# Kernel tuning notes

Measured on AMD Instinct MI355X. Metric: run time of the kernel, lower is better.

The kernel has to match this reference:

```python
import jax, jax.numpy as jnp
import numpy as np
import math

B, H, L, D = 2, 16, 2048, 128


def setup_inputs() -> dict:
    key = jax.random.key(0)
    kq, kk, kv, km, kp = jax.random.split(key, 5)
    q = jax.random.normal(kq, (B, H, L, D), dtype=jnp.float32)
    k = jax.random.normal(kk, (B, H, L, D), dtype=jnp.float32)
    v = jax.random.normal(kv, (B, H, L, D), dtype=jnp.float32)
    mask = jax.random.randint(km, (B, 1, L, L), 0, 2, dtype=jnp.int32)
    probs = jax.random.uniform(kp, (B, L, L), dtype=jnp.float32)
    alpha = jnp.ones((), dtype=jnp.float32)  # learned scalar Parameter, init 1.0
    return {"q": q, "k": k, "v": v, "mask": mask, "probs": probs, "alpha": alpha}


def reference(q, k, v, mask, probs, alpha):
    # scores: (B, H, L, L)
    scale = 1.0 / math.sqrt(q.shape[-1])
    attn_score = jnp.einsum("bhqd,bhkd->bhqk", q, k) * scale
    # additive learned-scale probability bias, broadcast over heads
    attn_score = attn_score + probs[:, None, :, :] * alpha
    # masked_fill(mask == 0, -inf)
    attn_score = jnp.where(mask == 0, -jnp.inf, attn_score)
    attn_p = jax.nn.softmax(attn_score, axis=-1)
    # dropout p=0.0 -> identity
    attention = jnp.einsum("bhqk,bhkd->bhqd", attn_p, v)
    return attention, attn_p
```

## Files before the change

### kernel.cpp

```cpp
#include <hip/hip_runtime.h>

constexpr int BB = 2, HH = 16, LL = 2048, DD = 128;
constexpr int QB = 64, KB = 32, NKT = LL / KB;
constexpr float SCALE = 0.08838834764831845f;

typedef __attribute__((ext_vector_type(8))) short bf16x8;
typedef __attribute__((ext_vector_type(8))) unsigned short u16x8;
typedef __attribute__((ext_vector_type(4))) float f32x4;
typedef __attribute__((ext_vector_type(4))) int i32x4;

static __device__ __forceinline__ unsigned short f2bf(float f) {
  unsigned int u = __builtin_bit_cast(unsigned int, f);
  u += 0x7fffu + ((u >> 16) & 1u);
  return (unsigned short)(u >> 16);
}
static __device__ __forceinline__ float bf2f(unsigned short h) {
  return __builtin_bit_cast(float, (unsigned int)h << 16);
}

#define GLD16(gsrc, ldst) __builtin_amdgcn_global_load_lds( \
    (const __attribute__((address_space(1))) void*)(gsrc), \
    (__attribute__((address_space(3))) void*)(ldst), 16, 0, 0)

__global__ __launch_bounds__(256)
void prep_kernel(const float* __restrict__ k, const float* __restrict__ v,
                 const int* __restrict__ mask, const float* __restrict__ probs,
                 const float* __restrict__ alphap,
                 unsigned short* __restrict__ kbT, unsigned short* __restrict__ vtT,
                 unsigned short* __restrict__ cpw)
{
  __shared__ unsigned short sT[128 * 40];
  const int bid = blockIdx.x;
  const int bh = bid >> 6, kt = bid & 63;
  const int t = threadIdx.x;
  const float alpha = alphap[0];
  const size_t tileBase = (size_t)bid * 4096;
  const float* kg = k + ((size_t)bh * LL + kt * 32) * DD;
  const float* vg = v + ((size_t)bh * LL + kt * 32) * DD;

  #pragma unroll
  for (int s = t; s < 512; s += 256) {
    int dsl = s >> 5, key = s & 31;
    const float* src = kg + key * DD + dsl * 8;
    float4 a = *(const float4*)src;
    float4 c = *(const float4*)(src + 4);
    u16x8 w;
    w[0] = f2bf(a.x); w[1] = f2bf(a.y); w[2] = f2bf(a.z); w[3] = f2bf(a.w);
    w[4] = f2bf(c.x); w[5] = f2bf(c.y); w[6] = f2bf(c.z); w[7] = f2bf(c.w);
    *(u16x8*)(kbT + tileBase + (size_t)s * 8) = w;
  }
  #pragma unroll
  for (int i = 0; i < 4; ++i) {
    int idx = i * 256 + t;
    int key = idx >> 5, d4 = (idx & 31) * 4;
    float4 x = ((const float4*)vg)[idx];
    sT[(d4 + 0) * 40 + key] = f2bf(x.x);
    sT[(d4 + 1) * 40 + key] = f2bf(x.y);
    sT[(d4 + 2) * 40 + key] = f2bf(x.z);
    sT[(d4 + 3) * 40 + key] = f2bf(x.w);
  }
  {
    const float4* ps = (const float4*)probs;
    const int4* ms = (const int4*)mask;
    ushort4* cs = (ushort4*)cpw;
    size_t base = (size_t)bid * 1024;
    #pragma unroll
    for (int i = 0; i < 4; ++i) {
      size_t idx = base + i * 256 + t;
      float4 p = ps[idx];
      int4 m = ms[idx];
      ushort4 o;
      o.x = f2bf(m.x ? p.x * alpha : -1e30f);
      o.y = f2bf(m.y ? p.y * alpha : -1e30f);
      o.z = f2bf(m.z ? p.z * alpha : -1e30f);
      o.w = f2bf(m.w ? p.w * alpha : -1e30f);
      cs[idx] = o;
    }
  }
  __syncthreads();
  #pragma unroll
  for (int s = t; s < 512; s += 256) {
    int kc = s >> 7, d = s & 127;
    u16x8 w = *(const u16x8*)&sT[d * 40 + kc * 8];
    *(u16x8*)(vtT + tileBase + (size_t)s * 8) = w;
  }
}

__global__ __launch_bounds__(256, 4)
void attn_kernel(const float* __restrict__ q, const unsigned short* __restrict__ kbT,
                 const unsigned short* __restrict__ vtT, const unsigned short* __restrict__ cpw,
                 float* __restrict__ outA, float* __restrict__ outP)
{
  __shared__ unsigned short sK[2][4096];
  __shared__ unsigned short sVt[2][4096];

  const int tid = threadIdx.x;
  const int lane = tid & 63;
  const int wid = tid >> 6;
  const int l15 = lane & 15;
  const int l4 = lane >> 4;

  const int bid = blockIdx.x;
  const int work = ((bid & 7) << 7) | (bid >> 3);
  const int bh = work >> 5;
  const int qt = work & 31;
  const int b = bh >> 4;
  const int q0 = qt * QB;
  const int row16 = wid << 4;

  const unsigned short* kbh = kbT + (size_t)bh * 64 * 4096;
  const unsigned short* vbh = vtT + (size_t)bh * 64 * 4096;
  const unsigned short* cgrow = cpw + (size_t)b * LL * LL + (size_t)(q0 + row16 + l15) * LL;
  float* oA = outA + (size_t)(bh * LL + q0) * DD;
  float* oPr = outP + (size_t)bh * LL * LL + (size_t)(q0 + row16 + l15) * LL;

  bf16x8 qf0, qf1, qf2, qf3;
  {
    const float* qs = q + (size_t)(bh * LL + q0 + row16 + l15) * DD + l4 * 8;
    #define LQ(FR, KC) { \
      float4 a = *(const float4*)(qs + (KC) * 32); \
      float4 c = *(const float4*)(qs + (KC) * 32 + 4); \
      FR[0]=(short)f2bf(a.x); FR[1]=(short)f2bf(a.y); FR[2]=(short)f2bf(a.z); FR[3]=(short)f2bf(a.w); \
      FR[4]=(short)f2bf(c.x); FR[5]=(short)f2bf(c.y); FR[6]=(short)f2bf(c.z); FR[7]=(short)f2bf(c.w); }
    LQ(qf0, 0) LQ(qf1, 1) LQ(qf2, 2) LQ(qf3, 3)
    #undef LQ
  }

  #define DMA_K(BUF, KT) do { \
    GLD16(kbh + (size_t)(KT) * 4096 + tid * 8,         &sK[BUF][wid << 9]); \
    GLD16(kbh + (size_t)(KT) * 4096 + (256 + tid) * 8, &sK[BUF][2048 + (wid << 9)]); } while (0)
  #define DMA_V(BUF, KT) do { \
    GLD16(vbh + (size_t)(KT) * 4096 + tid * 8,         &sVt[BUF][wid << 9]); \
    GLD16(vbh + (size_t)(KT) * 4096 + (256 + tid) * 8, &sVt[BUF][2048 + (wid << 9)]); } while (0)

  #define QKS(KC, QF) { \
    bf16x8 k0 = *(const bf16x8*)&sK[cur][(((KC) * 4 + l4) * 32 + l15) * 8]; \
    a0 = __builtin_amdgcn_mfma_f32_16x16x32_bf16(k0, QF, a0, 0, 0, 0); \
    bf16x8 k1 = *(const bf16x8*)&sK[cur][(((KC) * 4 + l4) * 32 + 16 + l15) * 8]; \
    a1 = __builtin_amdgcn_mfma_f32_16x16x32_bf16(k1, QF, a1, 0, 0, 0); }

  DMA_K(0, 0);
  ushort4 cn0 = *(const ushort4*)(cgrow + (l4 << 2));
  ushort4 cn1 = *(const ushort4*)(cgrow + 16 + (l4 << 2));
  float sum = 0.f;
  for (int kt = 0; kt < NKT; ++kt) {
    const int cur = kt & 1;
    __syncthreads();
    if (kt + 1 < NKT) DMA_K(cur ^ 1, kt + 1);
    ushort4 b0 = cn0, b1 = cn1;
    if (kt + 1 < NKT) {
      cn0 = *(const ushort4*)(cgrow + (kt + 1) * 32 + (l4 << 2));
      cn1 = *(const ushort4*)(cgrow + (kt + 1) * 32 + 16 + (l4 << 2));
    }
    f32x4 a0 = {0.f,0.f,0.f,0.f}, a1 = {0.f,0.f,0.f,0.f};
    QKS(0, qf0) QKS(1, qf1) QKS(2, qf2) QKS(3, qf3)
    sum += __expf(a0[0] * SCALE + bf2f(b0.x));
    sum += __expf(a0[1] * SCALE + bf2f(b0.y));
    sum += __expf(a0[2] * SCALE + bf2f(b0.z));
    sum += __expf(a0[3] * SCALE + bf2f(b0.w));
    sum += __expf(a1[0] * SCALE + bf2f(b1.x));
    sum += __expf(a1[1] * SCALE + bf2f(b1.y));
    sum += __expf(a1[2] * SCALE + bf2f(b1.z));
    sum += __expf(a1[3] * SCALE + bf2f(b1.w));
  }
  sum += __shfl_xor(sum, 16, 64);
  sum += __shfl_xor(sum, 32, 64);
  const float inv = 1.0f / sum;

  __syncthreads();
  DMA_K(0, 0); DMA_V(0, 0);
  cn0 = *(const ushort4*)(cgrow + (l4 << 2));
  cn1 = *(const ushort4*)(cgrow + 16 + (l4 << 2));
  f32x4 oacc[8];
  #pragma unroll
  for (int dt = 0; dt < 8; ++dt) oacc[dt] = (f32x4){0.f,0.f,0.f,0.f};

  const int srcA = l15 + (((l4 << 1) + 0) & 3) * 16;
  const int srcB = l15 + (((l4 << 1) + 1) & 3) * 16;
  const bool hiTile = (l4 >= 2);

  for (int kt = 0; kt < NKT; ++kt) {
    const int cur = kt & 1;
    __syncthreads();
    if (kt + 1 < NKT) { DMA_K(cur ^ 1, kt + 1); DMA_V(cur ^ 1, kt + 1); }
    ushort4 b0 = cn0, b1 = cn1;
    if (kt + 1 < NKT) {
      cn0 = *(const ushort4*)(cgrow + (kt + 1) * 32 + (l4 << 2));
      cn1 = *(const ushort4*)(cgrow + (kt + 1) * 32 + 16 + (l4 << 2));
    }
    f32x4 a0 = {0.f,0.f,0.f,0.f}, a1 = {0.f,0.f,0.f,0.f};
    QKS(0, qf0) QKS(1, qf1) QKS(2, qf2) QKS(3, qf3)

    f32x4 p0, p1;
    p0[0] = __expf(a0[0] * SCALE + bf2f(b0.x)) * inv;
    p0[1] = __expf(a0[1] * SCALE + bf2f(b0.y)) * inv;
    p0[2] = __expf(a0[2] * SCALE + bf2f(b0.z)) * inv;
    p0[3] = __expf(a0[3] * SCALE + bf2f(b0.w)) * inv;
    p1[0] = __expf(a1[0] * SCALE + bf2f(b1.x)) * inv;
    p1[1] = __expf(a1[1] * SCALE + bf2f(b1.y)) * inv;
    p1[2] = __expf(a1[2] * SCALE + bf2f(b1.z)) * inv;
    p1[3] = __expf(a1[3] * SCALE + bf2f(b1.w)) * inv;

    __builtin_nontemporal_store(p0, (f32x4*)(oPr + kt * 32 + (l4 << 2)));
    __builtin_nontemporal_store(p1, (f32x4*)(oPr + kt * 32 + 16 + (l4 << 2)));

    unsigned d00, d01, d10, d11;
    asm("v_cvt_pk_bf16_f32 %0, %1, %2" : "=v"(d00) : "v"(p0[0]), "v"(p0[1]));
    asm("v_cvt_pk_bf16_f32 %0, %1, %2" : "=v"(d01) : "v"(p0[2]), "v"(p0[3]));
    asm("v_cvt_pk_bf16_f32 %0, %1, %2" : "=v"(d10) : "v"(p1[0]), "v"(p1[1]));
    asm("v_cvt_pk_bf16_f32 %0, %1, %2" : "=v"(d11) : "v"(p1[2]), "v"(p1[3]));
    int a00 = __shfl((int)d00, srcA, 64);
    int a01 = __shfl((int)d01, srcA, 64);
    int a02 = __shfl((int)d00, srcB, 64);
    int a03 = __shfl((int)d01, srcB, 64);
    int b00 = __shfl((int)d10, srcA, 64);
    int b01 = __shfl((int)d11, srcA, 64);
    int b02 = __shfl((int)d10, srcB, 64);
    int b03 = __shfl((int)d11, srcB, 64);
    i32x4 fw;
    fw[0] = hiTile ? b00 : a00;
    fw[1] = hiTile ? b01 : a01;
    fw[2] = hiTile ? b02 : a02;
    fw[3] = hiTile ? b03 : a03;
    bf16x8 aP = __builtin_bit_cast(bf16x8, fw);

    #pragma unroll
    for (int dt = 0; dt < 8; ++dt) {
      bf16x8 bV = *(const bf16x8*)&sVt[cur][(l4 * 128 + dt * 16 + l15) * 8];
      oacc[dt] = __builtin_amdgcn_mfma_f32_16x16x32_bf16(aP, bV, oacc[dt], 0, 0, 0);
    }
  }

  #pragma unroll
  for (int dt = 0; dt < 8; ++dt) {
    #pragma unroll
    for (int r = 0; r < 4; ++r) {
      __builtin_nontemporal_store(oacc[dt][r],
          oA + (size_t)(row16 + (l4 << 2) + r) * DD + dt * 16 + l15);
    }
  }
}

extern "C" void kernel_launch(void* const* d_in, const int* in_sizes, int n_in,
                              void* d_out, int out_size, void* d_ws, size_t ws_size,
                              hipStream_t stream) {
  const float* q = (const float*)d_in[0];
  const float* k = (const float*)d_in[1];
  const float* v = (const float*)d_in[2];
  const int* mask = (const int*)d_in[3];
  const float* probs = (const float*)d_in[4];
  const float* alpha = (const float*)d_in[5];
  float* outA = (float*)d_out;
  float* outP = outA + (size_t)BB * HH * LL * DD;
  unsigned short* kbT = (unsigned short*)d_ws;
  unsigned short* vtT = kbT + (size_t)32 * 64 * 4096;
  unsigned short* cpw = vtT + (size_t)32 * 64 * 4096;
  hipLaunchKernelGGL(prep_kernel, dim3(32 * 64), dim3(256), 0, stream,
                     k, v, mask, probs, alpha, kbT, vtT, cpw);
  hipLaunchKernelGGL(attn_kernel, dim3(BB * HH * (LL / QB)), dim3(256), 0, stream,
                     q, kbT, vtT, cpw, outA, outP);
}
```

Measured before the change: 286.4 us.

## Split attention into separate row-sum pass and output pass kernels

Splits the fused two-pass attention kernel into two launches. The first computes softmax denominators from QK^T only, using less shared memory and a higher occupancy bound, and writes the inverse sums to workspace. The second reloads them and runs the probability and PV pass. This lets the lighter first pass run at higher occupancy, at the cost of an extra launch, reloading and reconverting Q, and a small extra global write and read.

Result: faster. 280.3 us (-2.1%).

```diff
diff --git a/kernel.cpp b/kernel.cpp
--- a/kernel.cpp
+++ b/kernel.cpp
@@ -86,13 +86,11 @@
   }
 }
 
-__global__ __launch_bounds__(256, 4)
-void attn_kernel(const float* __restrict__ q, const unsigned short* __restrict__ kbT,
-                 const unsigned short* __restrict__ vtT, const unsigned short* __restrict__ cpw,
-                 float* __restrict__ outA, float* __restrict__ outP)
+__global__ __launch_bounds__(256, 6)
+void passA_kernel(const float* __restrict__ q, const unsigned short* __restrict__ kbT,
+                  const unsigned short* __restrict__ cpw, float* __restrict__ invW)
 {
   __shared__ unsigned short sK[2][4096];
-  __shared__ unsigned short sVt[2][4096];
 
   const int tid = threadIdx.x;
   const int lane = tid & 63;
@@ -109,10 +107,7 @@
   const int row16 = wid << 4;
 
   const unsigned short* kbh = kbT + (size_t)bh * 64 * 4096;
-  const unsigned short* vbh = vtT + (size_t)bh * 64 * 4096;
   const unsigned short* cgrow = cpw + (size_t)b * LL * LL + (size_t)(q0 + row16 + l15) * LL;
-  float* oA = outA + (size_t)(bh * LL + q0) * DD;
-  float* oPr = outP + (size_t)bh * LL * LL + (size_t)(q0 + row16 + l15) * LL;
 
   bf16x8 qf0, qf1, qf2, qf3;
   {
@@ -129,9 +124,6 @@
   #define DMA_K(BUF, KT) do { \
     GLD16(kbh + (size_t)(KT) * 4096 + tid * 8,         &sK[BUF][wid << 9]); \
     GLD16(kbh + (size_t)(KT) * 4096 + (256 + tid) * 8, &sK[BUF][2048 + (wid << 9)]); } while (0)
-  #define DMA_V(BUF, KT) do { \
-    GLD16(vbh + (size_t)(KT) * 4096 + tid * 8,         &sVt[BUF][wid << 9]); \
-    GLD16(vbh + (size_t)(KT) * 4096 + (256 + tid) * 8, &sVt[BUF][2048 + (wid << 9)]); } while (0)
 
   #define QKS(KC, QF) { \
     bf16x8 k0 = *(const bf16x8*)&sK[cur][(((KC) * 4 + l4) * 32 + l15) * 8]; \
@@ -165,12 +157,71 @@
   }
   sum += __shfl_xor(sum, 16, 64);
   sum += __shfl_xor(sum, 32, 64);
-  const float inv = 1.0f / sum;
-
-  __syncthreads();
+  if (l4 == 0)
+    invW[(size_t)bh * LL + q0 + row16 + l15] = 1.0f / sum;
+  #undef DMA_K
+  #undef QKS
+}
+
+__global__ __launch_bounds__(256, 4)
+void passB_kernel(const float* __restrict__ q, const unsigned short* __restrict__ kbT,
+                  const unsigned short* __restrict__ vtT, const unsigned short* __restrict__ cpw,
+                  const float* __restrict__ invW,
+                  float* __restrict__ outA, float* __restrict__ outP)
+{
+  __shared__ unsigned short sK[2][4096];
+  __shared__ unsigned short sVt[2][4096];
+
+  const int tid = threadIdx.x;
+  const int lane = tid & 63;
+  const int wid = tid >> 6;
+  const int l15 = lane & 15;
+  const int l4 = lane >> 4;
+
+  const int bid = blockIdx.x;
+  const int work = ((bid & 7) << 7) | (bid >> 3);
+  const int bh = work >> 5;
+  const int qt = work & 31;
+  const int b = bh >> 4;
+  const int q0 = qt * QB;
+  const int row16 = wid << 4;
+
+  const unsigned short* kbh = kbT + (size_t)bh * 64 * 4096;
+  const unsigned short* vbh = vtT + (size_t)bh * 64 * 4096;
+  const unsigned short* cgrow = cpw + (size_t)b * LL * LL + (size_t)(q0 + row16 + l15) * LL;
+  float* oA = outA + (size_t)(bh * LL + q0) * DD;
+  float* oPr = outP + (size_t)bh * LL * LL + (size_t)(q0 + row16 + l15) * LL;
+
+  const float inv = invW[(size_t)bh * LL + q0 + row16 + l15];
+
+  bf16x8 qf0, qf1, qf2, qf3;
+  {
+    const float* qs = q + (size_t)(bh * LL + q0 + row16 + l15) * DD + l4 * 8;
+    #define LQ(FR, KC) { \
+      float4 a = *(const float4*)(qs + (KC) * 32); \
+      float4 c = *(const float4*)(qs + (KC) * 32 + 4); \
+      FR[0]=(short)f2bf(a.x); FR[1]=(short)f2bf(a.y); FR[2]=(short)f2bf(a.z); FR[3]=(short)f2bf(a.w); \
+      FR[4]=(short)f2bf(c.x); FR[5]=(short)f2bf(c.y); FR[6]=(short)f2bf(c.z); FR[7]=(short)f2bf(c.w); }
+    LQ(qf0, 0) LQ(qf1, 1) LQ(qf2, 2) LQ(qf3, 3)
+    #undef LQ
+  }
+
+  #define DMA_K(BUF, KT) do { \
+    GLD16(kbh + (size_t)(KT) * 4096 + tid * 8,         &sK[BUF][wid << 9]); \
+    GLD16(kbh + (size_t)(KT) * 4096 + (256 + tid) * 8, &sK[BUF][2048 + (wid << 9)]); } while (0)
+  #define DMA_V(BUF, KT) do { \
+    GLD16(vbh + (size_t)(KT) * 4096 + tid * 8,         &sVt[BUF][wid << 9]); \
+    GLD16(vbh + (size_t)(KT) * 4096 + (256 + tid) * 8, &sVt[BUF][2048 + (wid << 9)]); } while (0)
+
+  #define QKS(KC, QF) { \
+    bf16x8 k0 = *(const bf16x8*)&sK[cur][(((KC) * 4 + l4) * 32 + l15) * 8]; \
+    a0 = __builtin_amdgcn_mfma_f32_16x16x32_bf16(k0, QF, a0, 0, 0, 0); \
+    bf16x8 k1 = *(const bf16x8*)&sK[cur][(((KC) * 4 + l4) * 32 + 16 + l15) * 8]; \
+    a1 = __builtin_amdgcn_mfma_f32_16x16x32_bf16(k1, QF, a1, 0, 0, 0); }
+
   DMA_K(0, 0); DMA_V(0, 0);
-  cn0 = *(const ushort4*)(cgrow + (l4 << 2));
-  cn1 = *(const ushort4*)(cgrow + 16 + (l4 << 2));
+  ushort4 cn0 = *(const ushort4*)(cgrow + (l4 << 2));
+  ushort4 cn1 = *(const ushort4*)(cgrow + 16 + (l4 << 2));
   f32x4 oacc[8];
   #pragma unroll
   for (int dt = 0; dt < 8; ++dt) oacc[dt] = (f32x4){0.f,0.f,0.f,0.f};
@@ -255,8 +306,11 @@
   unsigned short* kbT = (unsigned short*)d_ws;
   unsigned short* vtT = kbT + (size_t)32 * 64 * 4096;
   unsigned short* cpw = vtT + (size_t)32 * 64 * 4096;
+  float* invW = (float*)(cpw + (size_t)BB * LL * LL);
   hipLaunchKernelGGL(prep_kernel, dim3(32 * 64), dim3(256), 0, stream,
                      k, v, mask, probs, alpha, kbT, vtT, cpw);
-  hipLaunchKernelGGL(attn_kernel, dim3(BB * HH * (LL / QB)), dim3(256), 0, stream,
-                     q, kbT, vtT, cpw, outA, outP);
-}
+  hipLaunchKernelGGL(passA_kernel, dim3(BB * HH * (LL / QB)), dim3(256), 0, stream,
+                     q, kbT, cpw, invW);
+  hipLaunchKernelGGL(passB_kernel, dim3(BB * HH * (LL / QB)), dim3(256), 0, stream,
+                     q, kbT, vtT, cpw, invW, outA, outP);
+}
```
